# Kernel tuning notes

Measured on AMD Instinct MI355X. Metric: run time of the kernel, lower is better.

Reference implementation:

```python
import jax, jax.numpy as jnp
import numpy as np

N, H, V = 8192, 2048, 32000
IGNORE_INDEX = -100


def setup_inputs() -> dict:
    key = jax.random.key(0)
    kx, kw, ky = jax.random.split(key, 3)
    x = jax.random.normal(kx, (N, H), dtype=jnp.float32)
    # nn.Linear weight layout: [out_features, in_features] = [V, H]
    W = jax.random.normal(kw, (V, H), dtype=jnp.float32) * (1.0 / np.sqrt(H))
    y = jax.random.randint(ky, (N,), 0, V, dtype=jnp.int64)
    return {"x": x, "W": W, "y": y}


def reference(x, W, y):
    # logits = x @ W.T : [N, V]  (the large tensor a fused kernel avoids)
    logits = jnp.einsum("nh,vh->nv", x, W)
    logp = jax.nn.log_softmax(logits, axis=-1)  # stable online log-softmax
    valid = y != IGNORE_INDEX
    y_safe = jnp.where(valid, y, 0)
    nll = -jnp.take_along_axis(logp, y_safe[:, None], axis=-1)[:, 0]  # [N]
    n_valid = jnp.sum(valid)
    # mean over non-ignored targets (Liger/torch CE 'mean' semantics)
    loss = jnp.sum(jnp.where(valid, nll, 0.0)) / jnp.maximum(n_valid, 1).astype(nll.dtype)
    return loss
```

## Files before the change

kernel.cpp:

```cpp
#include <hip/hip_runtime.h>
#include <stdint.h>

#define N_ROWS 8192
#define H_DIM  2048
#define V_DIM  32000
#define BM 256
#define BN 256
#define BK 64
#define NT (H_DIM / BK)
#define CT_NUM (V_DIM / BN)
#define RT_NUM (N_ROWS / BM)

typedef __attribute__((ext_vector_type(8))) short   short8;
typedef __attribute__((ext_vector_type(4))) float   f32x4;
typedef __attribute__((ext_vector_type(4))) float   v4f;
typedef __attribute__((ext_vector_type(4))) uint32_t v4u;

__device__ inline uint32_t f2bf(float f) {
    uint32_t u = __float_as_uint(f);
    return (u + 0x7fffu + ((u >> 16) & 1u)) >> 16;
}
__device__ inline float bf2f(uint16_t b) {
    return __uint_as_float(((uint32_t)b) << 16);
}

__device__ inline void gload_lds16(const void* g, void* l) {
    __builtin_amdgcn_global_load_lds(
        (const __attribute__((address_space(1))) void*)g,
        (__attribute__((address_space(3))) void*)l, 16, 0, 0);
}

__device__ __forceinline__ void stage_half(const uint16_t* g, char* l) {
    gload_lds16(g, l);
    gload_lds16(g + (size_t)64 * H_DIM, l + 8192);
}

__global__ void cvt_bf16(const float* __restrict__ src, uint16_t* __restrict__ dst, int n8) {
    int i = blockIdx.x * blockDim.x + threadIdx.x;
    if (i >= n8) return;
    v4f a = ((const v4f*)src)[(size_t)i * 2];
    v4f b = ((const v4f*)src)[(size_t)i * 2 + 1];
    uint32_t o0 = f2bf(a[0]) | (f2bf(a[1]) << 16);
    uint32_t o1 = f2bf(a[2]) | (f2bf(a[3]) << 16);
    uint32_t o2 = f2bf(b[0]) | (f2bf(b[1]) << 16);
    uint32_t o3 = f2bf(b[2]) | (f2bf(b[3]) << 16);
    ((v4u*)dst)[i] = (v4u){o0, o1, o2, o3};
}

__global__ __launch_bounds__(256) void ce_target(
    const uint16_t* __restrict__ xb, const uint16_t* __restrict__ wb,
    const int* __restrict__ y, float* __restrict__ t_logit)
{
    const int n    = blockIdx.x * 4 + (threadIdx.x >> 6);
    const int lane = threadIdx.x & 63;
    const int t    = y[n];
    float s = 0.f;
    if (t >= 0) {
        const uint16_t* xr = xb + (size_t)n * H_DIM;
        const uint16_t* wr = wb + (size_t)t * H_DIM;
#pragma unroll
        for (int j = 0; j < 4; ++j) {
            short8 a = *(const short8*)(xr + (lane + 64 * j) * 8);
            short8 b = *(const short8*)(wr + (lane + 64 * j) * 8);
#pragma unroll
            for (int e = 0; e < 8; ++e)
                s += bf2f((uint16_t)a[e]) * bf2f((uint16_t)b[e]);
        }
#pragma unroll
        for (int off = 1; off < 64; off <<= 1) s += __shfl_xor(s, off);
    }
    if (lane == 0) t_logit[n] = s;
}

__global__ __launch_bounds__(512, 2) void ce_gemm(
    const uint16_t* __restrict__ xb, const uint16_t* __restrict__ wb,
    float* __restrict__ l_part)
{
    extern __shared__ char lds[];

    const int tid = threadIdx.x;
    const int rb  = blockIdx.x;
    const int ct  = blockIdx.y;
    const int rowBase = rb * BM;
    const int colBase = ct * BN;

    const int lane = tid & 63;
    const int wave = tid >> 6;
    const int wm   = wave >> 2;
    const int wn   = wave & 3;
    const int quad = lane >> 4;
    const int l15  = lane & 15;

    f32x4 acc[8][4];
#pragma unroll
    for (int i = 0; i < 8; ++i)
#pragma unroll
        for (int j = 0; j < 4; ++j) acc[i][j] = (f32x4){0.f, 0.f, 0.f, 0.f};

    const int sr   = tid >> 3;
    const int slot = tid & 7;
    const int sc   = (slot ^ (sr & 7)) * 8;
    const uint16_t* gA = xb + (size_t)(rowBase + sr) * H_DIM + sc;
    const uint16_t* gB = wb + (size_t)(colBase + sr) * H_DIM + sc;
    char* lA = lds;
    char* lB = lds + 65536;

    const int aBase = (wm * 128 + l15) * 128;
    const int bBase = (wn * 64 + l15) * 128;
    int cOff[2];
#pragma unroll
    for (int kk = 0; kk < 2; ++kk)
        cOff[kk] = ((kk * 4 + quad) ^ (l15 & 7)) * 16;

    stage_half(gA,                         lA + tid * 16);
    stage_half(gA + (size_t)128 * H_DIM,   lA + 16384 + tid * 16);
    stage_half(gB,                         lB + tid * 16);
    stage_half(gB + (size_t)128 * H_DIM,   lB + 16384 + tid * 16);
    stage_half(gB + BK,                    lB + 32768 + tid * 16);
    stage_half(gB + (size_t)128 * H_DIM + BK, lB + 32768 + 16384 + tid * 16);
    asm volatile("s_waitcnt vmcnt(4)" ::: "memory");
    __builtin_amdgcn_s_barrier();

    for (int t = 0; t < NT; ++t) {
        const int c = t & 1;
        const char* bA = lA + c * 32768 + aBase;
        const char* bB = lB + c * 32768 + bBase;
        const int kA = (t + 1 < NT) ? (t + 1) * BK : 0;
        const int kB = (t + 2 < NT) ? (t + 2) * BK : 0;
        char* sA = lA + (c ^ 1) * 32768 + tid * 16;
        char* sB = lB + c * 32768 + tid * 16;

        short8 bfr[2][4];
#pragma unroll
        for (int p = 0; p < 4; ++p) {
            short8 af[2][2];
#pragma unroll
            for (int kk = 0; kk < 2; ++kk) {
                af[kk][0] = *(const short8*)(bA + (p * 2 + 0) * 2048 + cOff[kk]);
                af[kk][1] = *(const short8*)(bA + (p * 2 + 1) * 2048 + cOff[kk]);
            }
            if (p == 0) {
#pragma unroll
                for (int kk = 0; kk < 2; ++kk)
#pragma unroll
                    for (int ni = 0; ni < 4; ++ni)
                        bfr[kk][ni] = *(const short8*)(bB + ni * 2048 + cOff[kk]);
            }

            if (p == 0)      stage_half(gA + kA,                         sA);
            else if (p == 1) stage_half(gA + (size_t)128 * H_DIM + kA,   sA + 16384);
            else if (p == 2) stage_half(gB + kB,                         sB);
            else             stage_half(gB + (size_t)128 * H_DIM + kB,   sB + 16384);

            if (p == 3) asm volatile("s_waitcnt vmcnt(4)" ::: "memory");
            __builtin_amdgcn_s_barrier();
            asm volatile("s_waitcnt lgkmcnt(0)" ::: "memory");
            __builtin_amdgcn_sched_barrier(0);

            __builtin_amdgcn_s_setprio(1);
#pragma unroll
            for (int kk = 0; kk < 2; ++kk)
#pragma unroll
                for (int m = 0; m < 2; ++m)
#pragma unroll
                    for (int ni = 0; ni < 4; ++ni)
                        acc[p * 2 + m][ni] = __builtin_amdgcn_mfma_f32_16x16x32_bf16(
                            af[kk][m], bfr[kk][ni], acc[p * 2 + m][ni], 0, 0, 0);
            __builtin_amdgcn_s_setprio(0);
            __builtin_amdgcn_s_barrier();
        }
    }

    __syncthreads();

    float* red = (float*)lds;
#pragma unroll
    for (int mi = 0; mi < 8; ++mi) {
#pragma unroll
        for (int reg = 0; reg < 4; ++reg) {
            float s = __expf(acc[mi][0][reg]) + __expf(acc[mi][1][reg])
                    + __expf(acc[mi][2][reg]) + __expf(acc[mi][3][reg]);
            s += __shfl_xor(s, 1);
            s += __shfl_xor(s, 2);
            s += __shfl_xor(s, 4);
            s += __shfl_xor(s, 8);
            if (l15 == 0)
                red[wn * 256 + wm * 128 + mi * 16 + quad * 4 + reg] = s;
        }
    }
    __syncthreads();

    if (tid < BM)
        l_part[(size_t)ct * N_ROWS + rowBase + tid] =
            red[tid] + red[256 + tid] + red[512 + tid] + red[768 + tid];
}

__global__ void ce_rowreduce(const float* __restrict__ l_part,
                             const float* __restrict__ t_logit, const int* __restrict__ y,
                             float* __restrict__ partials)
{
    const int n = blockIdx.x * 256 + threadIdx.x;
    float l = 0.f;
    for (int ct = 0; ct < CT_NUM; ++ct) l += l_part[(size_t)ct * N_ROWS + n];

    const int t = y[n];
    float nll = 0.f, cnt = 0.f;
    if (t >= 0) { nll = __logf(l) - t_logit[n]; cnt = 1.f; }

#pragma unroll
    for (int off = 1; off < 64; off <<= 1) {
        nll += __shfl_xor(nll, off);
        cnt += __shfl_xor(cnt, off);
    }
    __shared__ float wred[8];
    const int wave = threadIdx.x >> 6, lane = threadIdx.x & 63;
    if (lane == 0) { wred[wave * 2] = nll; wred[wave * 2 + 1] = cnt; }
    __syncthreads();
    if (threadIdx.x == 0) {
        float s = 0.f, c = 0.f;
        for (int w = 0; w < 4; ++w) { s += wred[w * 2]; c += wred[w * 2 + 1]; }
        partials[blockIdx.x * 2]     = s;
        partials[blockIdx.x * 2 + 1] = c;
    }
}

__global__ void ce_final(const float* __restrict__ partials, float* __restrict__ out)
{
    const int t = threadIdx.x;
    float s = 0.f, c = 0.f;
    if (t < 32) { s = partials[t * 2]; c = partials[t * 2 + 1]; }
#pragma unroll
    for (int off = 1; off < 64; off <<= 1) { s += __shfl_xor(s, off); c += __shfl_xor(c, off); }
    if (t == 0) out[0] = s / fmaxf(c, 1.f);
}

extern "C" void kernel_launch(void* const* d_in, const int* in_sizes, int n_in,
                              void* d_out, int out_size, void* d_ws, size_t ws_size,
                              hipStream_t stream)
{
    const float* x = (const float*)d_in[0];
    const float* W = (const float*)d_in[1];
    const int*   y = (const int*)d_in[2];
    float*     out = (float*)d_out;

    char* ws = (char*)d_ws;
    uint16_t* xb      = (uint16_t*)(ws);
    uint16_t* wb      = (uint16_t*)(ws + 33554432);
    float*    l_part  = (float*)(ws + 164626432);
    float*    t_logit = (float*)(ws + 172818432);
    float*    partials= (float*)(ws + 172851200);

    {
        const int n8 = N_ROWS * H_DIM / 8;
        cvt_bf16<<<(n8 + 255) / 256, 256, 0, stream>>>(x, xb, n8);
    }
    {
        const int n8 = V_DIM * H_DIM / 8;
        cvt_bf16<<<(n8 + 255) / 256, 256, 0, stream>>>(W, wb, n8);
    }

    ce_target<<<N_ROWS / 4, 256, 0, stream>>>(xb, wb, y, t_logit);

    dim3 grid(RT_NUM, CT_NUM);
    ce_gemm<<<grid, 512, 131072, stream>>>(xb, wb, l_part);

    ce_rowreduce<<<N_ROWS / 256, 256, 0, stream>>>(l_part, t_logit, y, partials);
    ce_final<<<1, 64, 0, stream>>>(partials, out);
}
```

Measured before the change: 1.322 ms.

## Software-pipeline LDS fragment reads with MFMA using ping-pong register buffers

Restructures the GEMM main loop so that A and B fragment reads from LDS for the next sub-step run while the current MFMAs execute, using double register buffers (a0/a1, bE/bO) and unrolling by two tiles. It replaces the per-substep lgkmcnt(0) wait plus two barriers with two barriers per tile. The aim is to hide LDS latency and cut synchronisation overhead. The cost is higher VGPR pressure, which may lower occupancy, and the implicit waits on LDS reads are left to the compiler.

After: 1.254 ms. 5.1% less time.

```diff
diff --git a/kernel.cpp b/kernel.cpp
--- a/kernel.cpp
+++ b/kernel.cpp
@@ -112,63 +112,83 @@
     for (int kk = 0; kk < 2; ++kk)
         cOff[kk] = ((kk * 4 + quad) ^ (l15 & 7)) * 16;
 
-    stage_half(gA,                         lA + tid * 16);
-    stage_half(gA + (size_t)128 * H_DIM,   lA + 16384 + tid * 16);
-    stage_half(gB,                         lB + tid * 16);
-    stage_half(gB + (size_t)128 * H_DIM,   lB + 16384 + tid * 16);
-    stage_half(gB + BK,                    lB + 32768 + tid * 16);
+    short8 a0[2][2], a1[2][2];
+    short8 bE[2][4], bO[2][4];
+
+#define READA(DST, BASE, MI0)                                                  \
+    _Pragma("unroll")                                                          \
+    for (int kk = 0; kk < 2; ++kk) {                                           \
+        DST[kk][0] = *(const short8*)((BASE) + (MI0) * 2048 + cOff[kk]);       \
+        DST[kk][1] = *(const short8*)((BASE) + ((MI0) + 1) * 2048 + cOff[kk]); \
+    }
+
+#define READB(DST, BASE)                                                       \
+    _Pragma("unroll")                                                          \
+    for (int kk = 0; kk < 2; ++kk)                                             \
+        _Pragma("unroll")                                                      \
+        for (int ni = 0; ni < 4; ++ni)                                         \
+            DST[kk][ni] = *(const short8*)((BASE) + ni * 2048 + cOff[kk]);
+
+#define MFMA8(A, B, MB)                                                        \
+    __builtin_amdgcn_s_setprio(1);                                             \
+    _Pragma("unroll")                                                          \
+    for (int kk = 0; kk < 2; ++kk)                                             \
+        _Pragma("unroll")                                                      \
+        for (int m = 0; m < 2; ++m)                                            \
+            _Pragma("unroll")                                                  \
+            for (int ni = 0; ni < 4; ++ni)                                     \
+                acc[(MB) + m][ni] = __builtin_amdgcn_mfma_f32_16x16x32_bf16(   \
+                    A[kk][m], B[kk][ni], acc[(MB) + m][ni], 0, 0, 0);          \
+    __builtin_amdgcn_s_setprio(0);
+
+#define TILE(T, C, AC, AN, BCUR, BNXT)                                         \
+{                                                                              \
+    const char* bA  = lA + (C) * 32768 + aBase;                                \
+    const char* bAn = lA + ((C) ^ 1) * 32768 + aBase;                          \
+    const char* bBn = lB + ((C) ^ 1) * 32768 + bBase;                          \
+    const int kA = ((T) + 1 < NT) ? ((T) + 1) * BK : 0;                        \
+    const int kB = ((T) + 2 < NT) ? ((T) + 2) * BK : 0;                        \
+    char* sA = lA + ((C) ^ 1) * 32768 + tid * 16;                              \
+    char* sB = lB + (C) * 32768 + tid * 16;                                    \
+                         \
+    stage_half(gA + kA, sA);                                                   \
+    READA(AN, bA, 2);                                                          \
+    MFMA8(AC, BCUR, 0);                                                        \
+                                                                       \
+    stage_half(gA + (size_t)128 * H_DIM + kA, sA + 16384);                     \
+    READA(AC, bA, 4);                                                          \
+    MFMA8(AN, BCUR, 2);                                                        \
+    __builtin_amdgcn_s_barrier();              \
+    __builtin_amdgcn_sched_barrier(0);                                         \
+                   \
+    stage_half(gB + kB, sB);                                                   \
+    READA(AN, bA, 6);                                                          \
+    MFMA8(AC, BCUR, 4);                                                        \
+                                                                       \
+    stage_half(gB + (size_t)128 * H_DIM + kB, sB + 16384);                     \
+    MFMA8(AN, BCUR, 6);                                                        \
+    asm volatile("s_waitcnt vmcnt(4)" ::: "memory");                           \
+    __builtin_amdgcn_s_barrier();                  \
+    __builtin_amdgcn_sched_barrier(0);                                         \
+    READA(AC, bAn, 0);                                      \
+    READB(BNXT, bBn);                                 \
+}
+
+    stage_half(gA,                            lA + tid * 16);
+    stage_half(gA + (size_t)128 * H_DIM,      lA + 16384 + tid * 16);
+    stage_half(gB,                            lB + tid * 16);
+    stage_half(gB + (size_t)128 * H_DIM,      lB + 16384 + tid * 16);
+    stage_half(gB + BK,                       lB + 32768 + tid * 16);
     stage_half(gB + (size_t)128 * H_DIM + BK, lB + 32768 + 16384 + tid * 16);
     asm volatile("s_waitcnt vmcnt(4)" ::: "memory");
     __builtin_amdgcn_s_barrier();
-
-    for (int t = 0; t < NT; ++t) {
-        const int c = t & 1;
-        const char* bA = lA + c * 32768 + aBase;
-        const char* bB = lB + c * 32768 + bBase;
-        const int kA = (t + 1 < NT) ? (t + 1) * BK : 0;
-        const int kB = (t + 2 < NT) ? (t + 2) * BK : 0;
-        char* sA = lA + (c ^ 1) * 32768 + tid * 16;
-        char* sB = lB + c * 32768 + tid * 16;
-
-        short8 bfr[2][4];
-#pragma unroll
-        for (int p = 0; p < 4; ++p) {
-            short8 af[2][2];
-#pragma unroll
-            for (int kk = 0; kk < 2; ++kk) {
-                af[kk][0] = *(const short8*)(bA + (p * 2 + 0) * 2048 + cOff[kk]);
-                af[kk][1] = *(const short8*)(bA + (p * 2 + 1) * 2048 + cOff[kk]);
-            }
-            if (p == 0) {
-#pragma unroll
-                for (int kk = 0; kk < 2; ++kk)
-#pragma unroll
-                    for (int ni = 0; ni < 4; ++ni)
-                        bfr[kk][ni] = *(const short8*)(bB + ni * 2048 + cOff[kk]);
-            }
-
-            if (p == 0)      stage_half(gA + kA,                         sA);
-            else if (p == 1) stage_half(gA + (size_t)128 * H_DIM + kA,   sA + 16384);
-            else if (p == 2) stage_half(gB + kB,                         sB);
-            else             stage_half(gB + (size_t)128 * H_DIM + kB,   sB + 16384);
-
-            if (p == 3) asm volatile("s_waitcnt vmcnt(4)" ::: "memory");
-            __builtin_amdgcn_s_barrier();
-            asm volatile("s_waitcnt lgkmcnt(0)" ::: "memory");
-            __builtin_amdgcn_sched_barrier(0);
-
-            __builtin_amdgcn_s_setprio(1);
-#pragma unroll
-            for (int kk = 0; kk < 2; ++kk)
-#pragma unroll
-                for (int m = 0; m < 2; ++m)
-#pragma unroll
-                    for (int ni = 0; ni < 4; ++ni)
-                        acc[p * 2 + m][ni] = __builtin_amdgcn_mfma_f32_16x16x32_bf16(
-                            af[kk][m], bfr[kk][ni], acc[p * 2 + m][ni], 0, 0, 0);
-            __builtin_amdgcn_s_setprio(0);
-            __builtin_amdgcn_s_barrier();
-        }
+    __builtin_amdgcn_sched_barrier(0);
+    READA(a0, lA + aBase, 0);
+    READB(bE, lB + bBase);
+
+    for (int tt = 0; tt < NT; tt += 2) {
+        TILE(tt,     0, a0, a1, bE, bO);
+        TILE(tt + 1, 1, a0, a1, bO, bE);
     }
 
     __syncthreads();
```
